# Optimization experiments

Measured on AMD Instinct MI355X. Metric: run time of the kernel, lower is better.

The kernel has to match this reference:

```python
import jax, jax.numpy as jnp
import numpy as np

D_NODE, D_EDGE, D_MODEL, TOPK, N_HEADS = 64, 16, 256, 5, 4
HEAD_DIM = D_MODEL // N_HEADS


def setup_inputs() -> dict:
    key = jax.random.key(0)
    ks = jax.random.split(key, 24)
    B, N = 256, 512
    E = N - 1
    def lin(k, fi, fo):
        k1, k2 = jax.random.split(k)
        s = 1.0 / np.sqrt(fi)
        return (jax.random.uniform(k1, (fi, fo), jnp.float32, -s, s),
                jax.random.uniform(k2, (fo,), jnp.float32, -s, s))
    Wn, bn = lin(ks[0], 8, D_NODE)
    We, be = lin(ks[1], 3, D_EDGE)
    Wq, bq = lin(ks[2], D_NODE, D_MODEL)
    Wkv, bkv = lin(ks[3], 2 * D_NODE + D_EDGE, 2 * D_MODEL)
    # MultiheadAttention in/out projections (fixed shared weights)
    Wiq, biq = lin(ks[4], D_MODEL, D_MODEL)
    Wik, bik = lin(ks[5], D_MODEL, D_MODEL)
    Wiv, biv = lin(ks[6], D_MODEL, D_MODEL)
    Wo, bo = lin(ks[7], D_MODEL, D_MODEL)
    Wf1, bf1 = lin(ks[8], D_NODE + D_MODEL, D_MODEL)
    Wf2, bf2 = lin(ks[9], D_MODEL, D_MODEL)
    Ws1, bs1 = lin(ks[10], D_NODE + D_EDGE + D_MODEL, D_MODEL)
    Ws2, bs2 = lin(ks[11], D_MODEL, 1 + 6 * D_MODEL)
    node_raw = jax.random.normal(ks[12], (B, N, 8), jnp.float32)
    edge_raw = jax.random.normal(ks[13], (B, E, 3), jnp.float32)
    return dict(node_raw=node_raw, edge_raw=edge_raw, ego_id=0,
                Wn=Wn, bn=bn, We=We, be=be, Wq=Wq, bq=bq, Wkv=Wkv, bkv=bkv,
                Wiq=Wiq, biq=biq, Wik=Wik, bik=bik, Wiv=Wiv, biv=biv,
                Wo=Wo, bo=bo, Wf1=Wf1, bf1=bf1, Wf2=Wf2, bf2=bf2,
                Ws1=Ws1, bs1=bs1, Ws2=Ws2, bs2=bs2)


def reference(node_raw, edge_raw, ego_id,
              Wn, bn, We, be, Wq, bq, Wkv, bkv,
              Wiq, biq, Wik, bik, Wiv, biv, Wo, bo,
              Wf1, bf1, Wf2, bf2, Ws1, bs1, Ws2, bs2):
    B, N, _ = node_raw.shape
    E = N - 1
    ego_id = int(ego_id)
    idx = np.arange(N)
    neighbor_idx = jnp.asarray(idx[idx != ego_id])  # (E,)

    node_feat = node_raw @ Wn + bn                   # (B, N, d_node)
    edge_feat = edge_raw @ We + be                   # (B, E, d_edge)
    ego_feat = node_feat[:, ego_id]                  # (B, d_node)
    neighbor_feat = node_feat[:, neighbor_idx]       # (B, E, d_node)

    ego_bcast = jnp.broadcast_to(ego_feat[:, None, :], (B, E, D_NODE))
    edge_input = jnp.concatenate([ego_bcast, edge_feat, neighbor_feat], -1)

    Q = ego_feat @ Wq + bq                           # (B, d_model)
    kv = edge_input @ Wkv + bkv                      # (B, E, 2*d_model)
    K, V = kv[..., :D_MODEL], kv[..., D_MODEL:]

    # MultiheadAttention: single query per batch, E keys/values
    q = (Q @ Wiq + biq).reshape(B, N_HEADS, HEAD_DIM)
    k = (K @ Wik + bik).reshape(B, E, N_HEADS, HEAD_DIM)
    v = (V @ Wiv + biv).reshape(B, E, N_HEADS, HEAD_DIM)
    scores = jnp.einsum('bhd,behd->bhe', q, k) / np.sqrt(HEAD_DIM)
    attn = jax.nn.softmax(scores, axis=-1)           # (B, H, E)
    ctx = jnp.einsum('bhe,behd->bhd', attn, v).reshape(B, D_MODEL)
    c_ego = ctx @ Wo + bo                            # (B, d_model)

    h = jnp.concatenate([ego_feat, c_ego], -1)
    h_ego_prime = jax.nn.relu(h @ Wf1 + bf1) @ Wf2 + bf2  # (B, d_model)

    c_bcast = jnp.broadcast_to(c_ego[:, None, :], (B, E, D_MODEL))
    edge_input2 = jnp.concatenate([neighbor_feat, edge_feat, c_bcast], -1)
    score_out = jax.nn.relu(edge_input2 @ Ws1 + bs1) @ Ws2 + bs2  # (B,E,1+6*dm)
    score = score_out[..., 0]                        # (B, E)
    h_enc = score_out[..., 1:].reshape(B, E, 6, D_MODEL)

    topk_val, topk_idx = jax.lax.top_k(score, TOPK)  # (B, topk)
    selected = jnp.take_along_axis(h_enc, topk_idx[:, :, None, None], axis=1)
    alpha = jax.nn.softmax(topk_val, axis=-1)[:, :, None, None]  # (B,topk,1,1)
    selected = selected * alpha
    return h_ego_prime, selected, topk_idx, alpha
```

## Files before the change

kernel.cpp:

```cpp
#include <hip/hip_runtime.h>
#include <hip/hip_bf16.h>
#include <math.h>

constexpr int B = 256, NN = 512, EE = 511;

constexpr size_t F_NF    = 0;
constexpr size_t F_EF    = F_NF   + (size_t)B*NN*64;
constexpr size_t F_WCK   = F_EF   + (size_t)B*EE*16;
constexpr size_t F_BCK   = F_WCK  + 144*256;
constexpr size_t F_WCV   = F_BCK  + 256;
constexpr size_t F_BCV   = F_WCV  + 144*256;
constexpr size_t F_WQ2   = F_BCV  + 256;
constexpr size_t F_BQ2   = F_WQ2  + 64*256;
constexpr size_t F_Q     = F_BQ2  + 256;
constexpr size_t F_AW    = F_Q    + (size_t)B*256;
constexpr size_t F_C0    = F_AW   + (size_t)B*4*80;
constexpr size_t F_SC    = F_C0   + (size_t)B*4;
constexpr size_t F_US    = F_SC   + (size_t)B*4*EE;
constexpr size_t F_CEGO  = F_US   + (size_t)B*4*80;
constexpr size_t F_CVEC  = F_CEGO + (size_t)B*256;
constexpr size_t F_SC2   = F_CVEC + (size_t)B*256;
constexpr size_t F_ALPHA = F_SC2  + (size_t)B*EE;
constexpr size_t F_TKI   = F_ALPHA+ (size_t)B*5;
constexpr size_t F_HS    = F_SC;

constexpr size_t O_HEGO  = 0;
constexpr size_t O_SEL   = 65536;
constexpr size_t O_TKI   = 2031616;
constexpr size_t O_ALPHA = 2032896;

__global__ void k_fuse(const float* Wkv, const float* bkv, const float* Wik, const float* bik,
                       const float* Wiv, const float* biv, const float* Wq,  const float* bq,
                       const float* Wiq, const float* biq, float* ws){
  int t = blockIdx.x*256 + threadIdx.x;
  if (t < 36864){
    int r = t >> 8, c = t & 255;
    float a = 0.f;
    for (int m=0;m<256;m++) a += Wkv[(size_t)r*512+m] * Wik[(size_t)m*256+c];
    ws[F_WCK + t] = a;
  } else if (t < 37120){
    int c = t - 36864;
    float a = bik[c];
    for (int m=0;m<256;m++) a += bkv[m] * Wik[(size_t)m*256+c];
    ws[F_BCK + c] = a;
  } else if (t < 73984){
    int i = t - 37120; int r = i >> 8, c = i & 255;
    float a = 0.f;
    for (int m=0;m<256;m++) a += Wkv[(size_t)r*512+256+m] * Wiv[(size_t)m*256+c];
    ws[F_WCV + i] = a;
  } else if (t < 74240){
    int c = t - 73984;
    float a = biv[c];
    for (int m=0;m<256;m++) a += bkv[256+m] * Wiv[(size_t)m*256+c];
    ws[F_BCV + c] = a;
  } else if (t < 90624){
    int i = t - 74240; int r = i >> 8, c = i & 255;
    float a = 0.f;
    for (int m=0;m<256;m++) a += Wq[(size_t)r*256+m] * Wiq[(size_t)m*256+c];
    ws[F_WQ2 + i] = a;
  } else if (t < 90880){
    int c = t - 90624;
    float a = biq[c];
    for (int m=0;m<256;m++) a += bq[m] * Wiq[(size_t)m*256+c];
    ws[F_BQ2 + c] = a;
  }
}

__global__ void k_nf(const float* node_raw, const float* Wn, const float* bn, float* ws){
  size_t t = (size_t)blockIdx.x*256 + threadIdx.x;
  int j = (int)(t & 63); size_t row = t >> 6;
  float a = bn[j];
  #pragma unroll
  for (int i=0;i<8;i++) a += node_raw[row*8+i] * Wn[(size_t)i*64+j];
  ws[F_NF + t] = a;
}

__global__ void k_ef(const float* edge_raw, const float* We, const float* be, float* ws){
  size_t t = (size_t)blockIdx.x*256 + threadIdx.x;
  int j = (int)(t & 15); size_t row = t >> 4;
  float a = be[j];
  #pragma unroll
  for (int i=0;i<3;i++) a += edge_raw[row*3+i] * We[(size_t)i*16+j];
  ws[F_EF + t] = a;
}

__global__ void k_q(const int* ego_p, float* ws){
  int b = blockIdx.x, c = threadIdx.x;
  int ego = *ego_p;
  const float* egf = ws + F_NF + ((size_t)b*NN + ego)*64;
  const float* Wq2 = ws + F_WQ2;
  float a = ws[F_BQ2 + c];
  for (int i=0;i<64;i++) a += egf[i]*Wq2[(size_t)i*256+c];
  ws[F_Q + (size_t)b*256 + c] = a;
}

__global__ void k_head(const int* ego_p, float* ws){
  int b = blockIdx.x >> 2, h = blockIdx.x & 3;
  int tid = threadIdx.x;
  __shared__ float qh[64];
  __shared__ float red[256];
  if (tid < 64) qh[tid] = ws[F_Q + (size_t)b*256 + h*64 + tid];
  __syncthreads();
  const float* Wck = ws + F_WCK;
  float p = 0.f;
  size_t awbase = F_AW + ((size_t)(b*4+h))*80;
  if (tid < 64){
    const float* wr = Wck + (size_t)(80+tid)*256 + h*64;
    float a=0.f; for(int d=0;d<64;d++) a += wr[d]*qh[d];
    ws[awbase + tid] = a;
  } else if (tid < 80){
    int i = tid-64;
    const float* wr = Wck + (size_t)(64+i)*256 + h*64;
    float a=0.f; for(int d=0;d<64;d++) a += wr[d]*qh[d];
    ws[awbase + 64 + i] = a;
  } else if (tid < 144){
    int j = tid-80;
    const float* wr = Wck + (size_t)j*256 + h*64;
    float a=0.f; for(int d=0;d<64;d++) a += wr[d]*qh[d];
    int ego = *ego_p;
    p = ws[F_NF + ((size_t)b*NN+ego)*64 + j] * a;
  } else if (tid < 208){
    int d = tid-144;
    p = ws[F_BCK + h*64 + d] * qh[d];
  }
  red[tid]=p; __syncthreads();
  for (int s=128;s>0;s>>=1){ if(tid<s) red[tid]+=red[tid+s]; __syncthreads(); }
  if (tid==0) ws[F_C0 + b*4 + h] = red[0];
}

__global__ void k_scores(const int* ego_p, float* ws){
  int b = blockIdx.x, tid = threadIdx.x;
  __shared__ float awz[4][80];
  __shared__ float c0s[4];
  for (int l=tid; l<320; l+=256) awz[l/80][l%80] = ws[F_AW + (size_t)b*320 + l];
  if (tid<4) c0s[tid] = ws[F_C0 + b*4 + tid];
  __syncthreads();
  int ego = *ego_p;
  for (int e=tid; e<EE; e+=256){
    int node = e < ego ? e : e+1;
    const float4* nr = (const float4*)(ws + F_NF + ((size_t)b*NN+node)*64);
    const float4* er = (const float4*)(ws + F_EF + ((size_t)b*EE+e)*16);
    float s[4] = {c0s[0],c0s[1],c0s[2],c0s[3]};
    #pragma unroll
    for (int i=0;i<16;i++){
      float4 x = nr[i];
      #pragma unroll
      for (int h=0;h<4;h++)
        s[h] += x.x*awz[h][i*4] + x.y*awz[h][i*4+1] + x.z*awz[h][i*4+2] + x.w*awz[h][i*4+3];
    }
    #pragma unroll
    for (int i=0;i<4;i++){
      float4 x = er[i];
      #pragma unroll
      for (int h=0;h<4;h++)
        s[h] += x.x*awz[h][64+i*4] + x.y*awz[h][64+i*4+1] + x.z*awz[h][64+i*4+2] + x.w*awz[h][64+i*4+3];
    }
    #pragma unroll
    for (int h=0;h<4;h++) ws[F_SC + ((size_t)(b*4+h))*EE + e] = s[h]*0.125f;
  }
}

__global__ void k_softmax(float* ws){
  int bh = blockIdx.x, tid = threadIdx.x;
  float* s = ws + F_SC + (size_t)bh*EE;
  __shared__ float red[256];
  float v0 = tid<EE ? s[tid] : -INFINITY;
  float v1 = tid+256<EE ? s[tid+256] : -INFINITY;
  red[tid] = fmaxf(v0,v1); __syncthreads();
  for (int st=128;st>0;st>>=1){ if(tid<st) red[tid]=fmaxf(red[tid],red[tid+st]); __syncthreads(); }
  float m = red[0]; __syncthreads();
  float e0 = tid<EE ? expf(v0-m) : 0.f;
  float e1 = tid+256<EE ? expf(v1-m) : 0.f;
  red[tid] = e0+e1; __syncthreads();
  for (int st=128;st>0;st>>=1){ if(tid<st) red[tid]+=red[tid+st]; __syncthreads(); }
  float inv = 1.f/red[0];
  if (tid<EE) s[tid] = e0*inv;
  if (tid+256<EE) s[tid+256] = e1*inv;
}

__global__ void k_usum(const int* ego_p, float* ws){
  int b = blockIdx.x>>2, h = blockIdx.x&3, d = threadIdx.x;
  if (d >= 80) return;
  const float* at = ws + F_SC + ((size_t)(b*4+h))*EE;
  int ego = *ego_p;
  float a = 0.f;
  if (d < 64){
    const float* base = ws + F_NF + (size_t)b*NN*64 + d;
    for (int e=0;e<EE;e++){
      int node = e<ego?e:e+1;
      a += at[e]*base[(size_t)node*64];
    }
  } else {
    const float* base = ws + F_EF + (size_t)b*EE*16 + (d-64);
    for (int e=0;e<EE;e++) a += at[e]*base[(size_t)e*16];
  }
  ws[F_US + ((size_t)(b*4+h))*80 + d] = a;
}

__global__ void k_bfinal(const int* ego_p,
                         const float* Wo, const float* bo,
                         const float* Wf1, const float* bf1p,
                         const float* Wf2, const float* bf2p,
                         const float* Ws1, const float* bs1,
                         float* ws, float* out){
  int b = blockIdx.x, t = threadIdx.x;
  __shared__ float ego_s[64], us_s[4][80], ctx_s[256], cego_s[256], hf_s[256];
  int ego = *ego_p;
  if (t < 64) ego_s[t] = ws[F_NF + ((size_t)b*NN+ego)*64 + t];
  for (int l=t; l<320; l+=256) us_s[l/80][l%80] = ws[F_US + (size_t)b*320 + l];
  __syncthreads();
  {
    int h = t >> 6;
    const float* Wcv = ws + F_WCV;
    float a = ws[F_BCV + t];
    for (int i=0;i<64;i++) a += ego_s[i]*Wcv[(size_t)i*256+t];
    for (int i=0;i<16;i++) a += us_s[h][64+i]*Wcv[(size_t)(64+i)*256+t];
    for (int i=0;i<64;i++) a += us_s[h][i]*Wcv[(size_t)(80+i)*256+t];
    ctx_s[t]=a;
  }
  __syncthreads();
  {
    float a = bo[t];
    for (int i=0;i<256;i++) a += ctx_s[i]*Wo[(size_t)i*256+t];
    cego_s[t]=a; ws[F_CEGO + (size_t)b*256+t]=a;
  }
  __syncthreads();
  {
    float a = bf1p[t];
    for (int i=0;i<64;i++)  a += ego_s[i]*Wf1[(size_t)i*256+t];
    for (int i=0;i<256;i++) a += cego_s[i]*Wf1[(size_t)(64+i)*256+t];
    hf_s[t]=fmaxf(a,0.f);
  }
  __syncthreads();
  {
    float a = bf2p[t];
    for (int i=0;i<256;i++) a += hf_s[i]*Wf2[(size_t)i*256+t];
    out[O_HEGO + (size_t)b*256+t] = a;
  }
  {
    float a = bs1[t];
    for (int i=0;i<256;i++) a += cego_s[i]*Ws1[(size_t)(80+i)*256+t];
    ws[F_CVEC + (size_t)b*256+t]=a;
  }
}

__global__ __launch_bounds__(256) void k_bigscore(const int* ego_p, const float* Ws1,
                                                  const float* Ws2, const float* bs2, float* ws){
  int tile = blockIdx.x, b = blockIdx.y;
  int tid = threadIdx.x;
  __shared__ float Fe[64][80];
  __shared__ float cv_s[256], w2_s[256];
  cv_s[tid] = ws[F_CVEC + (size_t)b*256 + tid];
  w2_s[tid] = Ws2[(size_t)tid*1537];
  int ego = *ego_p;
  for (int l=tid; l<80*64; l+=256){
    int e = l/80, k = l - e*80;
    int eg = tile*64 + e;
    float v = 0.f;
    if (eg < EE){
      int node = eg<ego?eg:eg+1;
      v = (k<64) ? ws[F_NF + ((size_t)b*NN+node)*64 + k]
                 : ws[F_EF + ((size_t)b*EE+eg)*16 + (k-64)];
    }
    Fe[e][k] = v;
  }
  __syncthreads();
  int tc = tid & 31, te = tid >> 5;
  float acc[8][8];
  #pragma unroll
  for (int i=0;i<8;i++)
    #pragma unroll
    for (int j=0;j<8;j++) acc[i][j]=0.f;
  for (int k=0;k<80;k++){
    float av[8];
    #pragma unroll
    for (int i=0;i<8;i++) av[i] = Fe[te*8+i][k];
    float4 b0 = *(const float4*)(Ws1 + (size_t)k*256 + tc*8);
    float4 b1 = *(const float4*)(Ws1 + (size_t)k*256 + tc*8 + 4);
    float bv[8] = {b0.x,b0.y,b0.z,b0.w,b1.x,b1.y,b1.z,b1.w};
    #pragma unroll
    for (int i=0;i<8;i++)
      #pragma unroll
      for (int j=0;j<8;j++) acc[i][j] = fmaf(av[i], bv[j], acc[i][j]);
  }
  float bs20 = bs2[0];
  #pragma unroll
  for (int i=0;i<8;i++){
    float p = 0.f;
    #pragma unroll
    for (int j=0;j<8;j++){
      float hcol = acc[i][j] + cv_s[tc*8+j];
      p += fmaxf(hcol,0.f)*w2_s[tc*8+j];
    }
    #pragma unroll
    for (int m=16;m>0;m>>=1) p += __shfl_xor(p, m, 64);
    if (tc==0){
      int eg = tile*64 + te*8 + i;
      if (eg < EE) ws[F_SC2 + (size_t)b*EE + eg] = p + bs20;
    }
  }
}

__global__ void k_topk(float* ws, float* out){
  int b = blockIdx.x, tid = threadIdx.x;
  __shared__ float sv[256]; __shared__ int si[256];
  __shared__ float tv[8];   __shared__ int tix[8];
  const float* s = ws + F_SC2 + (size_t)b*EE;
  float v0 = tid<EE ? s[tid] : -INFINITY;       int i0 = tid;
  float v1 = (tid+256)<EE ? s[tid+256] : -INFINITY; int i1 = tid+256;
  for (int t=0;t<5;t++){
    float bvv; int bii;
    if (v0 > v1 || (v0==v1 && i0<i1)){ bvv=v0; bii=i0; } else { bvv=v1; bii=i1; }
    sv[tid]=bvv; si[tid]=bii; __syncthreads();
    for (int st=128; st>0; st>>=1){
      if (tid<st){
        float ov=sv[tid+st]; int oi=si[tid+st];
        if (ov > sv[tid] || (ov==sv[tid] && oi<si[tid])){ sv[tid]=ov; si[tid]=oi; }
      }
      __syncthreads();
    }
    if (tid==0){ tv[t]=sv[0]; tix[t]=si[0]; }
    __syncthreads();
    int w = tix[t];
    if (i0==w) v0=-INFINITY;
    if (i1==w) v1=-INFINITY;
    __syncthreads();
  }
  if (tid==0){
    float m = tv[0];
    float ex[5]; float sum=0.f;
    for (int t=0;t<5;t++){ ex[t]=expf(tv[t]-m); sum+=ex[t]; }
    for (int t=0;t<5;t++){
      float al = ex[t]/sum;
      ws[F_ALPHA + (size_t)b*5+t] = al;
      ((int*)(ws + F_TKI))[b*5+t] = tix[t];
      out[O_TKI   + (size_t)b*5+t] = (float)tix[t];
      out[O_ALPHA + (size_t)b*5+t] = al;
    }
  }
}

__global__ void k_hid(const int* ego_p, const float* Ws1, float* ws){
  int bt = blockIdx.x;
  int b = bt/5;
  int tid = threadIdx.x;
  __shared__ float fr[80];
  int e = ((const int*)(ws+F_TKI))[bt];
  int ego = *ego_p;
  int node = e<ego ? e : e+1;
  if (tid < 64)      fr[tid] = ws[F_NF + ((size_t)b*NN+node)*64 + tid];
  else if (tid < 80) fr[tid] = ws[F_EF + ((size_t)b*EE+e)*16 + (tid-64)];
  __syncthreads();
  float a = ws[F_CVEC + (size_t)b*256 + tid];
  for (int d=0;d<80;d++) a += fr[d]*Ws1[(size_t)d*256+tid];
  ws[F_HS + (size_t)bt*256 + tid] = fmaxf(a,0.f);
}

__global__ __launch_bounds__(256) void k_enc(const float* Ws2, const float* bs2,
                                             float* ws, float* out){
  int r = blockIdx.x, g = blockIdx.y, tid = threadIdx.x;
  int n = r*256 + tid;
  __shared__ float hs[10][256];
  __shared__ float al[10];
  int b0 = g*2;
  for (int l=tid; l<10*256; l+=256)
    hs[l>>8][l&255] = ws[F_HS + ((size_t)b0*5)*256 + l];
  if (tid<10) al[tid] = ws[F_ALPHA + (size_t)b0*5 + tid];
  __syncthreads();
  float acc[10];
  #pragma unroll
  for (int i=0;i<10;i++) acc[i]=0.f;
  const float* w2p = Ws2 + 1 + n;
  for (int j=0;j<256;j+=4){
    float w0 = w2p[(size_t)(j+0)*1537];
    float w1 = w2p[(size_t)(j+1)*1537];
    float w2 = w2p[(size_t)(j+2)*1537];
    float w3 = w2p[(size_t)(j+3)*1537];
    #pragma unroll
    for (int i=0;i<10;i++){
      float4 h = *(const float4*)&hs[i][j];
      acc[i] = fmaf(h.x,w0, fmaf(h.y,w1, fmaf(h.z,w2, fmaf(h.w,w3, acc[i]))));
    }
  }
  float bb = bs2[1+n];
  #pragma unroll
  for (int i=0;i<10;i++)
    out[O_SEL + ((size_t)(b0*5+i))*1536 + n] = (acc[i]+bb)*al[i];
}

extern "C" void kernel_launch(void* const* d_in, const int* in_sizes, int n_in,
                              void* d_out, int out_size, void* d_ws, size_t ws_size,
                              hipStream_t stream){
  const float* node_raw=(const float*)d_in[0];
  const float* edge_raw=(const float*)d_in[1];
  const int*  ego_p   =(const int*)d_in[2];
  const float* Wn =(const float*)d_in[3];  const float* bn =(const float*)d_in[4];
  const float* We =(const float*)d_in[5];  const float* be =(const float*)d_in[6];
  const float* Wq =(const float*)d_in[7];  const float* bq =(const float*)d_in[8];
  const float* Wkv=(const float*)d_in[9];  const float* bkv=(const float*)d_in[10];
  const float* Wiq=(const float*)d_in[11]; const float* biq=(const float*)d_in[12];
  const float* Wik=(const float*)d_in[13]; const float* bik=(const float*)d_in[14];
  const float* Wiv=(const float*)d_in[15]; const float* biv=(const float*)d_in[16];
  const float* Wo =(const float*)d_in[17]; const float* bo =(const float*)d_in[18];
  const float* Wf1=(const float*)d_in[19]; const float* bf1p=(const float*)d_in[20];
  const float* Wf2=(const float*)d_in[21]; const float* bf2p=(const float*)d_in[22];
  const float* Ws1=(const float*)d_in[23]; const float* bs1=(const float*)d_in[24];
  const float* Ws2=(const float*)d_in[25]; const float* bs2=(const float*)d_in[26];
  float* ws=(float*)d_ws;
  float* out=(float*)d_out;

  k_fuse<<<355,256,0,stream>>>(Wkv,bkv,Wik,bik,Wiv,biv,Wq,bq,Wiq,biq,ws);
  k_nf<<<(B*NN*64)/256,256,0,stream>>>(node_raw,Wn,bn,ws);
  k_ef<<<(B*EE*16)/256,256,0,stream>>>(edge_raw,We,be,ws);
  k_q<<<B,256,0,stream>>>(ego_p,ws);
  k_head<<<B*4,256,0,stream>>>(ego_p,ws);
  k_scores<<<B,256,0,stream>>>(ego_p,ws);
  k_softmax<<<B*4,256,0,stream>>>(ws);
  k_usum<<<B*4,128,0,stream>>>(ego_p,ws);
  k_bfinal<<<B,256,0,stream>>>(ego_p,Wo,bo,Wf1,bf1p,Wf2,bf2p,Ws1,bs1,ws,out);
  k_bigscore<<<dim3(8,B),256,0,stream>>>(ego_p,Ws1,Ws2,bs2,ws);
  k_topk<<<B,256,0,stream>>>(ws,out);
  k_hid<<<B*5,256,0,stream>>>(ego_p,Ws1,ws);
  k_enc<<<dim3(6,128),256,0,stream>>>(Ws2,bs2,ws,out);
}
```

Baseline: 289.5 us.

## Stage Ws1 tiles in shared memory and double threads in bigscore kernel

The score-hidden GEMM in k_bigscore now loads Ws1 in 16-row chunks into shared memory instead of reading each row from global memory per thread. The block grows to 512 threads, and each thread computes a 4x8 tile instead of 8x8, which cuts registers per thread and raises parallelism. A-operand reads from Fe become float4 loads. The cost is more __syncthreads per block and extra shared memory.

```diff
diff --git a/kernel.cpp b/kernel.cpp
--- a/kernel.cpp
+++ b/kernel.cpp
@@ -244,16 +244,19 @@
   }
 }
 
-__global__ __launch_bounds__(256) void k_bigscore(const int* ego_p, const float* Ws1,
+__global__ __launch_bounds__(512) void k_bigscore(const int* ego_p, const float* Ws1,
                                                   const float* Ws2, const float* bs2, float* ws){
   int tile = blockIdx.x, b = blockIdx.y;
   int tid = threadIdx.x;
   __shared__ float Fe[64][80];
+  __shared__ float Bs[16][256];
   __shared__ float cv_s[256], w2_s[256];
-  cv_s[tid] = ws[F_CVEC + (size_t)b*256 + tid];
-  w2_s[tid] = Ws2[(size_t)tid*1537];
-  int ego = *ego_p;
-  for (int l=tid; l<80*64; l+=256){
+  int ego = *ego_p;
+  if (tid < 256){
+    cv_s[tid] = ws[F_CVEC + (size_t)b*256 + tid];
+    w2_s[tid] = Ws2[(size_t)tid*1537];
+  }
+  for (int l=tid; l<80*64; l+=512){
     int e = l/80, k = l - e*80;
     int eg = tile*64 + e;
     float v = 0.f;
@@ -264,28 +267,45 @@
     }
     Fe[e][k] = v;
   }
-  __syncthreads();
   int tc = tid & 31, te = tid >> 5;
-  float acc[8][8];
-  #pragma unroll
-  for (int i=0;i<8;i++)
+  float acc[4][8];
+  #pragma unroll
+  for (int i=0;i<4;i++)
     #pragma unroll
     for (int j=0;j<8;j++) acc[i][j]=0.f;
-  for (int k=0;k<80;k++){
-    float av[8];
-    #pragma unroll
-    for (int i=0;i<8;i++) av[i] = Fe[te*8+i][k];
-    float4 b0 = *(const float4*)(Ws1 + (size_t)k*256 + tc*8);
-    float4 b1 = *(const float4*)(Ws1 + (size_t)k*256 + tc*8 + 4);
-    float bv[8] = {b0.x,b0.y,b0.z,b0.w,b1.x,b1.y,b1.z,b1.w};
-    #pragma unroll
-    for (int i=0;i<8;i++)
+
+  for (int c=0;c<5;c++){
+    __syncthreads();
+    {
+      float4* dst = (float4*)&Bs[0][0];
+      const float4* s4 = (const float4*)(Ws1 + (size_t)(c*16)*256);
+      dst[tid]       = s4[tid];
+      dst[tid + 512] = s4[tid + 512];
+    }
+    __syncthreads();
+    #pragma unroll
+    for (int kk=0; kk<16; kk+=4){
+      float A[4][4];
       #pragma unroll
-      for (int j=0;j<8;j++) acc[i][j] = fmaf(av[i], bv[j], acc[i][j]);
+      for (int i=0;i<4;i++){
+        float4 t4 = *(const float4*)&Fe[te*4+i][c*16+kk];
+        A[i][0]=t4.x; A[i][1]=t4.y; A[i][2]=t4.z; A[i][3]=t4.w;
+      }
+      #pragma unroll
+      for (int q=0;q<4;q++){
+        float4 b0 = *(const float4*)&Bs[kk+q][tc*8];
+        float4 b1 = *(const float4*)&Bs[kk+q][tc*8+4];
+        float bw[8] = {b0.x,b0.y,b0.z,b0.w,b1.x,b1.y,b1.z,b1.w};
+        #pragma unroll
+        for (int i=0;i<4;i++)
+          #pragma unroll
+          for (int j=0;j<8;j++) acc[i][j] = fmaf(A[i][q], bw[j], acc[i][j]);
+      }
+    }
   }
   float bs20 = bs2[0];
   #pragma unroll
-  for (int i=0;i<8;i++){
+  for (int i=0;i<4;i++){
     float p = 0.f;
     #pragma unroll
     for (int j=0;j<8;j++){
@@ -295,7 +315,7 @@
     #pragma unroll
     for (int m=16;m>0;m>>=1) p += __shfl_xor(p, m, 64);
     if (tc==0){
-      int eg = tile*64 + te*8 + i;
+      int eg = tile*64 + te*4 + i;
       if (eg < EE) ws[F_SC2 + (size_t)b*EE + eg] = p + bs20;
     }
   }
@@ -418,7 +438,7 @@
   k_softmax<<<B*4,256,0,stream>>>(ws);
   k_usum<<<B*4,128,0,stream>>>(ego_p,ws);
   k_bfinal<<<B,256,0,stream>>>(ego_p,Wo,bo,Wf1,bf1p,Wf2,bf2p,Ws1,bs1,ws,out);
-  k_bigscore<<<dim3(8,B),256,0,stream>>>(ego_p,Ws1,Ws2,bs2,ws);
+  k_bigscore<<<dim3(8,B),512,0,stream>>>(ego_p,Ws1,Ws2,bs2,ws);
   k_topk<<<B,256,0,stream>>>(ws,out);
   k_hid<<<B*5,256,0,stream>>>(ego_p,Ws1,ws);
   k_enc<<<dim3(6,128),256,0,stream>>>(Ws2,bs2,ws,out);
```

Result: no change. 287.7 us (-0.6%).
